# Optimization experiments

Measured on AMD Instinct MI355X. Metric: run time of the kernel, lower is better.

Reference implementation:

```python
import jax, jax.numpy as jnp
import numpy as np

SEQ = 4096
BLOCK = 64
NUM_RAND = 3
B, H, D = 1, 12, 64


def _build_bigbird_mask(seq_len=SEQ, block=BLOCK, num_rand=NUM_RAND, seed=0):
    """Dense [S,S] BigBird mask: global first/last block, window +-1 block,
    num_rand random blocks per middle row (mirrors bigbird_block_rand_mask)."""
    nb = seq_len // block
    rng = np.random.RandomState(seed)
    m = np.zeros((nb, nb), dtype=np.int32)
    # global blocks (first & last block attend/are attended everywhere)
    m[0, :] = 1
    m[-1, :] = 1
    m[:, 0] = 1
    m[:, -1] = 1
    # sliding window of one block on each side
    idx = np.arange(nb)
    win = np.abs(idx[:, None] - idx[None, :]) <= 1
    m[win] = 1
    # random blocks for middle rows, excluding window and global columns
    for i in range(1, nb - 1):
        cand = np.array([j for j in range(1, nb - 1) if abs(j - i) > 1], dtype=np.int32)
        sel = rng.permutation(cand)[:num_rand]
        m[i, sel] = 1
    return np.kron(m, np.ones((block, block), dtype=np.int32))


def setup_inputs() -> dict:
    key = jax.random.key(0)
    kq, kk, kv = jax.random.split(key, 3)
    q = jax.random.normal(kq, (B, H, SEQ, D), dtype=jnp.float32)
    k = jax.random.normal(kk, (B, H, SEQ, D), dtype=jnp.float32)
    v = jax.random.normal(kv, (B, H, SEQ, D), dtype=jnp.float32)
    mask = jnp.asarray(_build_bigbird_mask(), dtype=jnp.int32)  # [S, S]
    return {"q": q, "k": k, "v": v, "mask": mask}


def reference(q, k, v, mask):
    # OriginalFullAttention with dense BigBird mask:
    # scores = QK^T / sqrt(D); masked positions get -10000 additive bias.
    scale = 1.0 / np.sqrt(D).astype(np.float32)
    scores = jnp.einsum("bhqd,bhkd->bhqk", q, k) * scale
    adder = (1.0 - mask.astype(scores.dtype)) * jnp.asarray(-10000.0, scores.dtype)
    probs = jax.nn.softmax(scores + adder[None, None, :, :], axis=-1)
    out = jnp.einsum("bhqk,bhkd->bhqd", probs, v)  # [B, H, S, D]
    return out
```

## Files before the change

### kernel.cpp

```cpp
#include <hip/hip_runtime.h>
#include <stdint.h>

#define SEQ 4096
#define DH  64
#define NB  64
#define NH  12

typedef float  f32x4   __attribute__((ext_vector_type(4)));
typedef float  f32x16  __attribute__((ext_vector_type(16)));
typedef short  s16x8   __attribute__((ext_vector_type(8)));
typedef unsigned short ushort_t;
typedef unsigned long long u64;

__device__ __forceinline__ unsigned short f2bf(float x){
    union { float f; unsigned u; } c; c.f = x;
    unsigned u = c.u;
    u += 0x7fffu + ((u >> 16) & 1u);
    return (unsigned short)(u >> 16);
}

__device__ __forceinline__ unsigned cvtpk(float lo, float hi){
    unsigned r;
    asm("v_cvt_pk_bf16_f32 %0, %1, %2" : "=v"(r) : "v"(lo), "v"(hi));
    return r;
}

__device__ __forceinline__ s16x8 pack8(f32x4 a, f32x4 b){
    s16x8 r;
#pragma unroll
    for (int i = 0; i < 4; ++i) { r[i] = (short)f2bf(a[i]); r[i+4] = (short)f2bf(b[i]); }
    return r;
}

__device__ __forceinline__ int swz(int row, int col){
    return row * 64 + (col ^ ((row & 7) << 3));
}

#define GLOAD_LDS(gp, lp) __builtin_amdgcn_global_load_lds( \
    (const __attribute__((address_space(1))) unsigned int*)(gp), \
    (__attribute__((address_space(3))) unsigned int*)(lp), 16, 0, 0)

#define KBF_OFF   0
#define VTB_OFF   6291456
#define PART_OFF  12582912
#define BMP_OFF   15777792
#define WS_NEED   15778304
#define SLOT_F    4160

__global__ __launch_bounds__(256) void bb_conv(
        const float* __restrict__ k, const float* __restrict__ v,
        const int* __restrict__ mask,
        ushort_t* __restrict__ kbf, ushort_t* __restrict__ vtb,
        u64* __restrict__ bmp)
{
    const int lin = blockIdx.x;
    const int job = (lin & 7) * 96 + (lin >> 3);
    const int h   = job >> 6;
    const int kb  = job & 63;
    const int tid = threadIdx.x;
    __shared__ float vls[64*65];

    if (h == 0 && tid < 64){
        bool a = mask[(size_t)(kb*64)*SEQ + tid*64] != 0;
        u64 bm = __ballot(a);
        if (tid == 0) bmp[kb] = bm;
    }

    const int j = tid >> 2, c = (tid & 3) * 16;
    const size_t gsrc = (size_t)h*SEQ*DH + (size_t)(kb*64 + j)*DH + c;
    const size_t tdst = ((size_t)h*NB + kb) * 4096;

    {
        f32x4 a0 = *(const f32x4*)(k + gsrc);
        f32x4 a1 = *(const f32x4*)(k + gsrc + 4);
        f32x4 a2 = *(const f32x4*)(k + gsrc + 8);
        f32x4 a3 = *(const f32x4*)(k + gsrc + 12);
        *(s16x8*)&kbf[tdst + swz(j, c    )] = pack8(a0, a1);
        *(s16x8*)&kbf[tdst + swz(j, c + 8)] = pack8(a2, a3);
    }
    {
        f32x4 b0 = *(const f32x4*)(v + gsrc);
        f32x4 b1 = *(const f32x4*)(v + gsrc + 4);
        f32x4 b2 = *(const f32x4*)(v + gsrc + 8);
        f32x4 b3 = *(const f32x4*)(v + gsrc + 12);
#pragma unroll
        for (int i = 0; i < 4; ++i){
            vls[j*65 + c + i     ] = b0[i];
            vls[j*65 + c + 4 + i ] = b1[i];
            vls[j*65 + c + 8 + i ] = b2[i];
            vls[j*65 + c + 12 + i] = b3[i];
        }
    }
    __syncthreads();
    {
        const int d = tid >> 2, jc = (tid & 3) * 16;
        s16x8 r0, r1;
#pragma unroll
        for (int i = 0; i < 8; ++i){
            r0[i] = (short)f2bf(vls[(jc + i    )*65 + d]);
            r1[i] = (short)f2bf(vls[(jc + i + 8)*65 + d]);
        }
        const int f0 = ((jc >> 5) << 2) + (((jc >> 4) & 1) << 1) + (d >> 5);
        *(s16x8*)&vtb[tdst + f0*512 +       (d & 31)*8] = r0;
        *(s16x8*)&vtb[tdst + f0*512 + 256 + (d & 31)*8] = r1;
    }
}

__global__ __launch_bounds__(256) void bb_main(
        const float* __restrict__ q,
        const ushort_t* __restrict__ kbf, const ushort_t* __restrict__ vtb,
        const u64* __restrict__ bmp,
        float* __restrict__ out, float* __restrict__ part)
{
    const int lin = blockIdx.x;
    const int job = (lin & 7) * 117 + (lin >> 3);
    const int h   = job / 78;
    const int x   = job - h * 78;

    int qb, wq = -1, sp = 0; u64 rmask;
    if (x < 62) { qb = x + 1; rmask = ~0ull; }
    else { int e = x - 62; wq = e >> 3; sp = e & 7; qb = wq ? 63 : 0; rmask = 0xFFull << (sp*8); }

    const int tid  = threadIdx.x;
    const int wave = tid >> 6;
    const int lane = tid & 63;
    const int l31  = lane & 31;
    const int hi   = lane >> 5;
    const int qh   = wave >> 1;
    const int kh   = wave & 1;

    __shared__ __align__(16) ushort_t KV[2][4096];
    __shared__ float lsm[64];

    const size_t hoff = (size_t)h * SEQ * DH;

    s16x8 qf[4];
    {
        const float sc = 0.125f * 1.4426950408889634f;
        const float* qp = q + hoff + (size_t)(qb*64 + qh*32 + l31) * DH + 8*hi;
#pragma unroll
        for (int c = 0; c < 4; ++c){
            f32x4 a = *(const f32x4*)(qp + c*16);
            f32x4 b = *(const f32x4*)(qp + c*16 + 4);
            a *= sc; b *= sc;
            qf[c] = pack8(a, b);
        }
    }

    u64 bits = bmp[qb] & rmask;

    const ushort_t* Kb = kbf + (size_t)h * (NB*4096);
    const ushort_t* Vb = vtb + (size_t)h * (NB*4096);

    f32x16 oa0 = {0.f}, oa1 = {0.f};
    float lp = 0.f;

    const int soff = wave*1024 + lane*16;
#define STAGE(gbase, lbase)                                          \
    {                                                                \
        const char* g0 = (const char*)(gbase) + soff;                \
        char*       l0 = (char*)(lbase) + wave*1024;                 \
        GLOAD_LDS(g0, l0);                                           \
        GLOAD_LDS(g0 + 4096, l0 + 4096);                             \
    }

    if (bits){
        const int n = __popcll(bits);
        u64 rem = bits;

        const int kb0 = __builtin_ctzll(rem); rem &= rem - 1;
        STAGE(Kb + (size_t)kb0*4096, &KV[0][0]);

        int kb_cur = kb0;
        int buf = 0;
        for (int t = 0; t < n; ++t){
            asm volatile("s_waitcnt vmcnt(0)" ::: "memory");
            __builtin_amdgcn_s_barrier();

            const ushort_t* vp = Vb + (size_t)kb_cur*4096 + kh*2048 + lane*8;
            s16x8 vf00 = *(const s16x8*)(vp       );
            s16x8 vf01 = *(const s16x8*)(vp +  512);
            s16x8 vf10 = *(const s16x8*)(vp + 1024);
            s16x8 vf11 = *(const s16x8*)(vp + 1536);

            int kbn = kb0;
            if (rem){ kbn = __builtin_ctzll(rem); rem &= rem - 1; }
            STAGE(Kb + (size_t)kbn*4096, &KV[buf^1][0]);

            const ushort_t* Kt = &KV[buf][0];

            f32x16 sa = {0.f};
            __builtin_amdgcn_s_setprio(1);
#pragma unroll
            for (int c = 0; c < 4; ++c){
                s16x8 kf = *(const s16x8*)&Kt[swz(kh*32 + l31, c*16 + 8*hi)];
                sa = __builtin_amdgcn_mfma_f32_32x32x16_bf16(kf, qf[c], sa, 0, 0, 0);
            }
            __builtin_amdgcn_s_setprio(0);

            float p[16];
#pragma unroll
            for (int r = 0; r < 16; ++r){
                p[r] = __builtin_amdgcn_exp2f(sa[r]);
                lp += p[r];
            }

            s16x8 pa[2];
#pragma unroll
            for (int s = 0; s < 2; ++s){
                unsigned a1 = cvtpk(p[8*s+0], p[8*s+1]);
                unsigned b1 = cvtpk(p[8*s+4], p[8*s+5]);
                unsigned a2 = cvtpk(p[8*s+2], p[8*s+3]);
                unsigned b2 = cvtpk(p[8*s+6], p[8*s+7]);
                asm("v_permlane32_swap_b32 %0, %1" : "+v"(a1), "+v"(b1));
                asm("v_permlane32_swap_b32 %0, %1" : "+v"(a2), "+v"(b2));
                union { unsigned w[4]; s16x8 v; } u;
                u.w[0] = a1; u.w[1] = a2; u.w[2] = b1; u.w[3] = b2;
                pa[s] = u.v;
            }

            __builtin_amdgcn_s_setprio(1);
            oa0 = __builtin_amdgcn_mfma_f32_32x32x16_bf16(pa[0], vf00, oa0, 0, 0, 0);
            oa1 = __builtin_amdgcn_mfma_f32_32x32x16_bf16(pa[0], vf01, oa1, 0, 0, 0);
            oa0 = __builtin_amdgcn_mfma_f32_32x32x16_bf16(pa[1], vf10, oa0, 0, 0, 0);
            oa1 = __builtin_amdgcn_mfma_f32_32x32x16_bf16(pa[1], vf11, oa1, 0, 0, 0);
            __builtin_amdgcn_s_setprio(0);

            kb_cur = kbn;
            buf ^= 1;
        }
    }
#undef STAGE

    float lpf = lp + __shfl_xor(lp, 32);

    __syncthreads();
    float* msm = (float*)&KV[0][0];

    if (kh == 1){
#pragma unroll
        for (int r = 0; r < 16; ++r){
            const int o = (qh*32 + ((r&3) + 8*(r>>2) + 4*hi)) * 64;
            msm[o +      l31] = oa0[r];
            msm[o + 32 + l31] = oa1[r];
        }
        if (lane < 32) lsm[qh*32 + lane] = lpf;
    }
    __syncthreads();

    if (kh == 0){
#pragma unroll
        for (int r = 0; r < 16; ++r){
            const int o = (qh*32 + ((r&3) + 8*(r>>2) + 4*hi)) * 64;
            msm[o +      l31] += oa0[r];
            msm[o + 32 + l31] += oa1[r];
        }
        if (lane < 32){
            float lt = lpf + lsm[qh*32 + lane];
            lsm[qh*32 + lane] = (wq < 0) ? (lt > 0.f ? 1.0f / lt : 0.f) : lt;
        }
    }
    __syncthreads();

    const size_t obase = hoff + (size_t)(qb*64) * DH;

    if (wq < 0){
#pragma unroll
        for (int i = 0; i < 4; ++i){
            const int idx = i*1024 + tid*4;
            f32x4 vv = *(const f32x4*)&msm[idx];
            vv *= lsm[idx >> 6];
            *(f32x4*)&out[obase + idx] = vv;
        }
    } else {
        float* pp = part + ((size_t)(h*2 + wq)*8 + sp) * SLOT_F;
#pragma unroll
        for (int i = 0; i < 4; ++i){
            const int idx = i*1024 + tid*4;
            *(f32x4*)&pp[idx] = *(const f32x4*)&msm[idx];
        }
        if (tid < 64) pp[4096 + tid] = lsm[tid];
    }
}

__global__ __launch_bounds__(256) void bb_comb(
        const float* __restrict__ part, float* __restrict__ out)
{
    const int h = blockIdx.x >> 1, wq = blockIdx.x & 1;
    const int qb = wq ? 63 : 0;
    const int tid = threadIdx.x;
    const int i = tid >> 2, cg = (tid & 3) * 16;

    const float* base = part + (size_t)(h*2 + wq) * 8 * SLOT_F;
    f32x4 acc[4] = {{0,0,0,0},{0,0,0,0},{0,0,0,0},{0,0,0,0}};
    float ls = 0.f;
#pragma unroll
    for (int s = 0; s < 8; ++s){
        const float* p = base + (size_t)s * SLOT_F;
#pragma unroll
        for (int c4 = 0; c4 < 4; ++c4)
            acc[c4] += *(const f32x4*)(p + (size_t)i*DH + cg + c4*4);
        ls += p[4096 + i];
    }
    const float inv = ls > 0.f ? 1.0f / ls : 0.f;
    float* op = out + (size_t)h*SEQ*DH + (size_t)(qb*64 + i)*DH + cg;
#pragma unroll
    for (int c4 = 0; c4 < 4; ++c4){
        f32x4 r = acc[c4] * inv;
        *(f32x4*)(op + c4*4) = r;
    }
}

__global__ __launch_bounds__(256) void bb_attn_fb(
        const float* __restrict__ q, const float* __restrict__ k,
        const float* __restrict__ v, const int* __restrict__ mask,
        float* __restrict__ out)
{
    const int qb   = blockIdx.x;
    const int h    = blockIdx.y;
    const int tid  = threadIdx.x;
    const int wave = tid >> 6;
    const int lane = tid & 63;
    const int lrow = lane & 15;
    const int lgrp = lane >> 4;

    __shared__ __align__(16) ushort_t Kb[64*64];
    __shared__ __align__(16) ushort_t Vt[64*64];
    __shared__ __align__(16) ushort_t Pw[4][16*64];

    const size_t hoff = (size_t)h * SEQ * DH;
    const int qrow = qb*64 + wave*16 + lrow;
    const float* qp = q + hoff + (size_t)qrow * DH + lgrp*8;
    s16x8 qf[2];
#pragma unroll
    for (int kc = 0; kc < 2; ++kc){
        f32x4 a = *(const f32x4*)(qp + kc*32);
        f32x4 b = *(const f32x4*)(qp + kc*32 + 4);
        a *= 0.125f; b *= 0.125f;
        qf[kc] = pack8(a, b);
    }
    const f32x4 zero = {0.f,0.f,0.f,0.f};
    f32x4 oa[4] = {zero, zero, zero, zero};
    float m_run[4] = {-1e30f,-1e30f,-1e30f,-1e30f};
    float l_run[4] = {0.f,0.f,0.f,0.f};
    const int* mrow = mask + (size_t)(qb*64) * SEQ;
    const int kr  = tid >> 2, kcg  = tid & 3;
    const int j2  = tid >> 3, dgrp = tid & 7;

    for (int kb = 0; kb < NB; ++kb){
        if (mrow[kb*64] == 0) continue;
        __syncthreads();
        {
            const float* kp = k + hoff + (size_t)(kb*64 + kr) * DH + kcg*16;
            f32x4 a0 = *(const f32x4*)(kp);
            f32x4 a1 = *(const f32x4*)(kp+4);
            f32x4 a2 = *(const f32x4*)(kp+8);
            f32x4 a3 = *(const f32x4*)(kp+12);
            *(s16x8*)&Kb[(kr*64) + (kcg*16     ^ ((kr&7)<<3))] = pack8(a0, a1);
            *(s16x8*)&Kb[(kr*64) + ((kcg*16+8) ^ ((kr&7)<<3))] = pack8(a2, a3);
        }
        {
            const float* vp0 = v + hoff + (size_t)(kb*64 + 2*j2) * DH + dgrp*8;
            f32x4 b0 = *(const f32x4*)(vp0);
            f32x4 b1 = *(const f32x4*)(vp0+4);
            f32x4 b2 = *(const f32x4*)(vp0+DH);
            f32x4 b3 = *(const f32x4*)(vp0+DH+4);
            float r0[8] = {b0[0],b0[1],b0[2],b0[3],b1[0],b1[1],b1[2],b1[3]};
            float r1[8] = {b2[0],b2[1],b2[2],b2[3],b3[0],b3[1],b3[2],b3[3]};
#pragma unroll
            for (int i = 0; i < 8; ++i){
                int dd = (i + dgrp) & 7;
                int d  = dgrp*8 + dd;
                unsigned val = (unsigned)f2bf(r0[dd]) | ((unsigned)f2bf(r1[dd]) << 16);
                *(unsigned*)&Vt[(d*64) + (2*j2 ^ ((d&7)<<3))] = val;
            }
        }
        __syncthreads();
        f32x4 sa[4] = {zero, zero, zero, zero};
#pragma unroll
        for (int jt = 0; jt < 4; ++jt)
#pragma unroll
            for (int kc = 0; kc < 2; ++kc){
                int row = jt*16 + lrow, col = kc*32 + lgrp*8;
                s16x8 kf = *(const s16x8*)&Kb[row*64 + (col ^ ((row&7)<<3))];
                sa[jt] = __builtin_amdgcn_mfma_f32_16x16x32_bf16(qf[kc], kf, sa[jt], 0, 0, 0);
            }
        float fac[4];
#pragma unroll
        for (int r = 0; r < 4; ++r){
            float mx = fmaxf(fmaxf(sa[0][r], sa[1][r]), fmaxf(sa[2][r], sa[3][r]));
            mx = fmaxf(mx, __shfl_xor(mx, 1));
            mx = fmaxf(mx, __shfl_xor(mx, 2));
            mx = fmaxf(mx, __shfl_xor(mx, 4));
            mx = fmaxf(mx, __shfl_xor(mx, 8));
            float mn = fmaxf(m_run[r], mx);
            fac[r] = __expf(m_run[r] - mn);
            m_run[r] = mn;
        }
#pragma unroll
        for (int r = 0; r < 4; ++r){
            float p0 = __expf(sa[0][r] - m_run[r]);
            float p1 = __expf(sa[1][r] - m_run[r]);
            float p2 = __expf(sa[2][r] - m_run[r]);
            float p3 = __expf(sa[3][r] - m_run[r]);
            sa[0][r]=p0; sa[1][r]=p1; sa[2][r]=p2; sa[3][r]=p3;
            float sm = p0+p1+p2+p3;
            sm += __shfl_xor(sm, 1);
            sm += __shfl_xor(sm, 2);
            sm += __shfl_xor(sm, 4);
            sm += __shfl_xor(sm, 8);
            l_run[r] = l_run[r]*fac[r] + sm;
        }
#pragma unroll
        for (int dc = 0; dc < 4; ++dc)
#pragma unroll
            for (int r = 0; r < 4; ++r) oa[dc][r] *= fac[r];
#pragma unroll
        for (int jt = 0; jt < 4; ++jt)
#pragma unroll
            for (int r = 0; r < 4; ++r){
                int row = lgrp*4 + r, col = jt*16 + lrow;
                Pw[wave][row*64 + (col ^ ((row&7)<<3))] = f2bf(sa[jt][r]);
            }
        s16x8 pf0 = *(const s16x8*)&Pw[wave][lrow*64 + ((     lgrp*8) ^ ((lrow&7)<<3))];
        s16x8 pf1 = *(const s16x8*)&Pw[wave][lrow*64 + ((32 + lgrp*8) ^ ((lrow&7)<<3))];
#pragma unroll
        for (int dc = 0; dc < 4; ++dc){
            int row0 = dc*16 + lrow;
            s16x8 v0 = *(const s16x8*)&Vt[row0*64 + ((     lgrp*8) ^ ((row0&7)<<3))];
            s16x8 v1 = *(const s16x8*)&Vt[row0*64 + ((32 + lgrp*8) ^ ((row0&7)<<3))];
            oa[dc] = __builtin_amdgcn_mfma_f32_16x16x32_bf16(pf0, v0, oa[dc], 0, 0, 0);
            oa[dc] = __builtin_amdgcn_mfma_f32_16x16x32_bf16(pf1, v1, oa[dc], 0, 0, 0);
        }
    }
    float inv[4];
#pragma unroll
    for (int r = 0; r < 4; ++r) inv[r] = 1.0f / l_run[r];
    float* op = out + hoff + (size_t)(qb*64 + wave*16) * DH;
#pragma unroll
    for (int dc = 0; dc < 4; ++dc)
#pragma unroll
        for (int r = 0; r < 4; ++r)
            op[(size_t)(lgrp*4 + r) * DH + dc*16 + lrow] = oa[dc][r] * inv[r];
}

extern "C" void kernel_launch(void* const* d_in, const int* in_sizes, int n_in,
                              void* d_out, int out_size, void* d_ws, size_t ws_size,
                              hipStream_t stream)
{
    const float* q    = (const float*)d_in[0];
    const float* k    = (const float*)d_in[1];
    const float* v    = (const float*)d_in[2];
    const int*   mask = (const int*)d_in[3];
    float* out = (float*)d_out;

    if (ws_size < (size_t)WS_NEED){
        dim3 grid(NB, NH, 1);
        bb_attn_fb<<<grid, 256, 0, stream>>>(q, k, v, mask, out);
        return;
    }

    char* ws = (char*)d_ws;
    ushort_t* kbf = (ushort_t*)(ws + KBF_OFF);
    ushort_t* vtb = (ushort_t*)(ws + VTB_OFF);
    float*    prt = (float*)   (ws + PART_OFF);
    u64*      bmp = (u64*)     (ws + BMP_OFF);

    bb_conv<<<dim3(768, 1, 1), 256, 0, stream>>>(k, v, mask, kbf, vtb, bmp);
    bb_main<<<dim3(936, 1, 1), 256, 0, stream>>>(q, kbf, vtb, bmp, out, prt);
    bb_comb<<<dim3(24, 1, 1), 256, 0, stream>>>(prt, out);
}
```

Before: 36.14 us.

## Stage K per wave into private LDS buffers to drop per-iteration barrier

```diff
diff --git a/kernel.cpp b/kernel.cpp
--- a/kernel.cpp
+++ b/kernel.cpp
@@ -129,8 +129,7 @@
     const int qh   = wave >> 1;
     const int kh   = wave & 1;
 
-    __shared__ __align__(16) ushort_t KV[2][4096];
-    __shared__ float lsm[64];
+    __shared__ __align__(16) ushort_t KW[4][2][2048];
 
     const size_t hoff = (size_t)h * SEQ * DH;
 
@@ -155,13 +154,15 @@
     f32x16 oa0 = {0.f}, oa1 = {0.f};
     float lp = 0.f;
 
-    const int soff = wave*1024 + lane*16;
-#define STAGE(gbase, lbase)                                          \
-    {                                                                \
-        const char* g0 = (const char*)(gbase) + soff;                \
-        char*       l0 = (char*)(lbase) + wave*1024;                 \
-        GLOAD_LDS(g0, l0);                                           \
-        GLOAD_LDS(g0 + 4096, l0 + 4096);                             \
+#define STAGE(kbidx, b)                                                   \
+    {                                                                     \
+        const char* g0 = (const char*)(Kb + (size_t)(kbidx)*4096)         \
+                         + kh*4096 + lane*16;                             \
+        char* l0 = (char*)&KW[wave][b][0] + lane*16;                      \
+        GLOAD_LDS(g0,        l0       );                                  \
+        GLOAD_LDS(g0 + 1024, l0 + 1024);                                  \
+        GLOAD_LDS(g0 + 2048, l0 + 2048);                                  \
+        GLOAD_LDS(g0 + 3072, l0 + 3072);                                  \
     }
 
     if (bits){
@@ -169,13 +170,12 @@
         u64 rem = bits;
 
         const int kb0 = __builtin_ctzll(rem); rem &= rem - 1;
-        STAGE(Kb + (size_t)kb0*4096, &KV[0][0]);
+        STAGE(kb0, 0);
 
         int kb_cur = kb0;
         int buf = 0;
         for (int t = 0; t < n; ++t){
             asm volatile("s_waitcnt vmcnt(0)" ::: "memory");
-            __builtin_amdgcn_s_barrier();
 
             const ushort_t* vp = Vb + (size_t)kb_cur*4096 + kh*2048 + lane*8;
             s16x8 vf00 = *(const s16x8*)(vp       );
@@ -183,17 +183,19 @@
             s16x8 vf10 = *(const s16x8*)(vp + 1024);
             s16x8 vf11 = *(const s16x8*)(vp + 1536);
 
-            int kbn = kb0;
-            if (rem){ kbn = __builtin_ctzll(rem); rem &= rem - 1; }
-            STAGE(Kb + (size_t)kbn*4096, &KV[buf^1][0]);
-
-            const ushort_t* Kt = &KV[buf][0];
+            if (rem){
+                int kbn = __builtin_ctzll(rem); rem &= rem - 1;
+                STAGE(kbn, buf^1);
+                kb_cur = kbn;
+            }
+
+            const ushort_t* Kt = &KW[wave][buf][0];
 
             f32x16 sa = {0.f};
             __builtin_amdgcn_s_setprio(1);
 #pragma unroll
             for (int c = 0; c < 4; ++c){
-                s16x8 kf = *(const s16x8*)&Kt[swz(kh*32 + l31, c*16 + 8*hi)];
+                s16x8 kf = *(const s16x8*)&Kt[l31*64 + ((c*16 + 8*hi) ^ ((l31 & 7) << 3))];
                 sa = __builtin_amdgcn_mfma_f32_32x32x16_bf16(kf, qf[c], sa, 0, 0, 0);
             }
             __builtin_amdgcn_s_setprio(0);
@@ -226,7 +228,6 @@
             oa1 = __builtin_amdgcn_mfma_f32_32x32x16_bf16(pa[1], vf11, oa1, 0, 0, 0);
             __builtin_amdgcn_s_setprio(0);
 
-            kb_cur = kbn;
             buf ^= 1;
         }
     }
@@ -234,8 +235,10 @@
 
     float lpf = lp + __shfl_xor(lp, 32);
 
+    asm volatile("s_waitcnt vmcnt(0)" ::: "memory");
     __syncthreads();
-    float* msm = (float*)&KV[0][0];
+    float* msm = (float*)&KW[0][0][0];
+    float* lsm = (float*)&KW[2][0][0];
 
     if (kh == 1){
 #pragma unroll
```

Result: no change. 36.44 us (+0.8%).
